# Kernel tuning notes

Hardware: AMD Instinct MI355X
Metric: run time of the kernel (lower is better)

## Reference

```python
import jax, jax.numpy as jnp
import numpy as np

N_NODES = 50000
N_EDGES = 800000
E_DIM = 128
N_LAYERS = 3
IN_DIM = 2
OUT_DIM = 1


def _lin_init(key, fan_in, fan_out, scale=None):
    # rough kaiming-tanh init, exact values don't matter for correctness testing
    s = scale if scale is not None else (5.0 / 3.0) / np.sqrt(fan_in)
    return jax.random.normal(key, (fan_in, fan_out), dtype=jnp.float32) * s


def setup_inputs() -> dict:
    key = jax.random.key(0)
    ks = jax.random.split(key, 16)
    node_feature = jax.random.normal(ks[0], (N_NODES, IN_DIM), dtype=jnp.float32)
    edge_index = jax.random.randint(ks[1], (2, N_EDGES), 0, N_NODES)
    batch = jnp.zeros((N_NODES,), dtype=jnp.int32)

    enc_W = _lin_init(ks[2], IN_DIM, E_DIM)
    enc_b = jnp.zeros((E_DIM,), dtype=jnp.float32)

    def stack(k, fan_in, fan_out):
        kk = jax.random.split(k, N_LAYERS)
        return jnp.stack([_lin_init(kk[i], fan_in, fan_out) for i in range(N_LAYERS)])

    gate_W = stack(ks[3], E_DIM, E_DIM)
    gate_b = jnp.zeros((N_LAYERS, E_DIM), dtype=jnp.float32)
    att_W = stack(ks[4], E_DIM, E_DIM)
    att_b = jnp.zeros((N_LAYERS, E_DIM), dtype=jnp.float32)
    msg_W = stack(ks[5], E_DIM, E_DIM)
    msg_b = jnp.zeros((N_LAYERS, E_DIM), dtype=jnp.float32)
    upd_W = stack(ks[6], 2 * E_DIM, E_DIM)
    upd_b = jnp.zeros((N_LAYERS, E_DIM), dtype=jnp.float32)

    dec1_W = _lin_init(ks[7], E_DIM, E_DIM // 2)
    dec1_b = jnp.zeros((E_DIM // 2,), dtype=jnp.float32)
    dec2_W = _lin_init(ks[8], E_DIM // 2, OUT_DIM, scale=1.0 / np.sqrt(E_DIM // 2))
    dec2_b = jnp.zeros((OUT_DIM,), dtype=jnp.float32)

    return dict(node_feature=node_feature, edge_index=edge_index, batch=batch,
                enc_W=enc_W, enc_b=enc_b,
                gate_W=gate_W, gate_b=gate_b, att_W=att_W, att_b=att_b,
                msg_W=msg_W, msg_b=msg_b, upd_W=upd_W, upd_b=upd_b,
                dec1_W=dec1_W, dec1_b=dec1_b, dec2_W=dec2_W, dec2_b=dec2_b)


def _segment_softmax(x, seg, num_segments):
    # PyG softmax over segments, numerically stable, per-channel
    m = jax.ops.segment_max(x, seg, num_segments=num_segments)
    m = jnp.where(jnp.isfinite(m), m, 0.0)
    e = jnp.exp(x - m[seg])
    s = jax.ops.segment_sum(e, seg, num_segments=num_segments)
    return e / (s[seg] + 1e-16)


def reference(node_feature, edge_index, batch,
              enc_W, enc_b, gate_W, gate_b, att_W, att_b,
              msg_W, msg_b, upd_W, upd_b,
              dec1_W, dec1_b, dec2_W, dec2_b):
    n = node_feature.shape[0]
    src, dst = edge_index[0], edge_index[1]  # j -> i (source_to_target)
    h = jnp.tanh(node_feature @ enc_W + enc_b)  # [N, E_DIM]
    for l in range(N_LAYERS):
        mj = jnp.tanh(h[src] @ msg_W[l] + msg_b[l])          # messages [Edges, E_DIM]
        gate = mj @ gate_W[l] + gate_b[l]                     # gate_nn (Linear only)
        alpha = _segment_softmax(gate, dst, n)                # softmax over incoming edges
        v = jnp.tanh(mj @ att_W[l] + att_b[l])                # attention_mlp
        aggr = jax.ops.segment_sum(alpha * v, dst, num_segments=n)
        h = jnp.tanh(jnp.concatenate([h, aggr], axis=1) @ upd_W[l] + upd_b[l])
    out = jnp.tanh(h @ dec1_W + dec1_b)
    out = out @ dec2_W + dec2_b
    return out
```

## Files before the change

kernel.cpp:

```cpp
#include <hip/hip_runtime.h>
#include <math.h>

#define ED 128
#define PROW 256

typedef _Float16 f16;
typedef _Float16 half8 __attribute__((ext_vector_type(8)));
typedef _Float16 half4 __attribute__((ext_vector_type(4)));
typedef _Float16 half2v __attribute__((ext_vector_type(2)));
typedef float f32x4 __attribute__((ext_vector_type(4)));

static __device__ __forceinline__ float tanh_fast(float x) {
  float ax = fabsf(x);
  float e = __expf(2.0f * ax);
  float t = 1.0f - 2.0f / (e + 1.0f);
  return __builtin_copysignf(t, x);
}

template <int NT, int NBYTES>
static __device__ __forceinline__ void stage256(
    const char* __restrict__ gsrc, char* lds, int tid) {
  #pragma unroll
  for (int i = 0; i < NBYTES / (NT * 16); ++i) {
    int b = (i * NT + tid) * 16;
    int row = b >> 8;
    int sw = (b & 255) ^ ((row & 7) << 4);
    float4 v = *reinterpret_cast<const float4*>(gsrc + (size_t)row * 256 + sw);
    *reinterpret_cast<float4*>(lds + b) = v;
  }
}

static __device__ __forceinline__ half8 read_w(const char* Wsb, int col, int koff) {
  int byte = col * 256 + (koff ^ ((col & 7) << 4));
  return *reinterpret_cast<const half8*>(Wsb + byte);
}

template <int NT>
static __device__ __forceinline__ void stage512(
    const char* __restrict__ gsrc, char* lds, int tid) {
  #pragma unroll
  for (int i = 0; i < 32768 / (NT * 16); ++i) {
    int b = (i * NT + tid) * 16;
    int row = b >> 9;
    int sw = (b & 511) ^ ((row & 7) << 4);
    float4 v = *reinterpret_cast<const float4*>(gsrc + (size_t)row * 512 + sw);
    *reinterpret_cast<float4*>(lds + b) = v;
  }
}

static __device__ __forceinline__ half8 read_w512(const char* Wsb, int colL, int koff) {
  int byte = colL * 512 + (koff ^ ((colL & 7) << 4));
  return *reinterpret_cast<const half8*>(Wsb + byte);
}

__global__ __launch_bounds__(256) void encoder_kernel(
    const float* __restrict__ x, const float* __restrict__ W,
    const float* __restrict__ b, f16* __restrict__ h, int n) {
  int idx = blockIdx.x * blockDim.x + threadIdx.x;
  if (idx >= n * ED) return;
  int i = idx >> 7, c = idx & 127;
  float v = x[i * 2 + 0] * W[c] + x[i * 2 + 1] * W[ED + c] + b[c];
  h[idx] = (f16)tanh_fast(v);
}

__global__ __launch_bounds__(256) void transpose_w_kernel(
    const float* __restrict__ src, f16* __restrict__ dst, int K, int C, int total) {
  int idx = blockIdx.x * 256 + threadIdx.x;
  if (idx >= total) return;
  int kc = K * C;
  int m = idx / kc;
  int rem = idx - m * kc;
  int c = rem / K;
  int k = rem - c * K;
  dst[idx] = (f16)src[(size_t)m * kc + (size_t)k * C + c];
}

__global__ __launch_bounds__(256) void transpose3_kernel(
    const float* __restrict__ s0, const float* __restrict__ s1,
    const float* __restrict__ s2, f16* __restrict__ d0,
    f16* __restrict__ d1, f16* __restrict__ d2) {
  int idx = blockIdx.x * 256 + threadIdx.x;
  const int per = 3 * 128 * 128;
  int which = idx / per;
  if (which >= 3) return;
  int rem = idx - which * per;
  const float* s = (which == 0) ? s0 : (which == 1) ? s1 : s2;
  f16* d = (which == 0) ? d0 : (which == 1) ? d1 : d2;
  int m = rem >> 14;
  int r2 = rem & 16383;
  int c = r2 >> 7, k = r2 & 127;
  d[rem] = (f16)s[m * 16384 + k * 128 + c];
}

__global__ __launch_bounds__(256) void count_deg_kernel(
    const int* __restrict__ dst, int* __restrict__ deg, int E) {
  int e = blockIdx.x * blockDim.x + threadIdx.x;
  if (e < E) atomicAdd(&deg[dst[e]], 1);
}

__global__ __launch_bounds__(1024) void scan_kernel(
    const int* __restrict__ deg, int* __restrict__ offs,
    int* __restrict__ cursor, int n) {
  __shared__ int wsum[16];
  __shared__ int carry_s;
  const int tid = threadIdx.x;
  const int lane = tid & 63;
  const int wid = tid >> 6;
  if (tid == 0) carry_s = 0;
  __syncthreads();
  for (int base = 0; base < n; base += 1024) {
    const int i = base + tid;
    const int v = (i < n) ? deg[i] : 0;
    int x = v;
    #pragma unroll
    for (int d = 1; d < 64; d <<= 1) {
      int t = __shfl_up(x, d, 64);
      if (lane >= d) x += t;
    }
    if (lane == 63) wsum[wid] = x;
    __syncthreads();
    int wbase = 0, total = 0;
    #pragma unroll
    for (int w = 0; w < 16; ++w) {
      int s = wsum[w];
      if (w < wid) wbase += s;
      total += s;
    }
    const int carry = carry_s;
    if (i < n) {
      const int excl = carry + wbase + x - v;
      offs[i] = excl;
      cursor[i] = excl;
    }
    __syncthreads();
    if (tid == 0) carry_s = carry + total;
    __syncthreads();
  }
  if (tid == 0) offs[n] = carry_s;
}

__global__ __launch_bounds__(256) void scatter_kernel(
    const int* __restrict__ src, const int* __restrict__ dst,
    int* __restrict__ cursor, int* __restrict__ ssrc, int E) {
  int e = blockIdx.x * blockDim.x + threadIdx.x;
  if (e < E) {
    int d = dst[e];
    int pos = atomicAdd(&cursor[d], 1);
    ssrc[pos] = src[e];
  }
}


__global__ __launch_bounds__(512, 4) void gemm_mgv_kernel(
    const f16* __restrict__ h,
    const f16* __restrict__ mWt, const float* __restrict__ mb,
    const f16* __restrict__ gWt, const float* __restrict__ gb,
    const f16* __restrict__ aWt, const float* __restrict__ ab,
    f16* __restrict__ P, int n) {
  __shared__ f16 Ws[128 * 128];
  __shared__ f16 Ss[128 * 128];
  char* Wsb = reinterpret_cast<char*>(Ws);
  char* Sb = reinterpret_cast<char*>(Ss);
  const int tid = threadIdx.x;
  const int wd = tid >> 6, lane = tid & 63;
  const int lr = lane & 15, lg = lane >> 4;
  const int r0 = blockIdx.x * 128 + wd * 16;

  half8 a[4];
  {
    int rr = r0 + lr;
    if (rr >= n) rr = n - 1;
    const f16* ap = h + (size_t)rr * ED + lg * 8;
    #pragma unroll
    for (int kt = 0; kt < 4; ++kt)
      a[kt] = *reinterpret_cast<const half8*>(ap + kt * 32);
  }

  stage256<512, 32768>((const char*)mWt, Wsb, tid);
  __syncthreads();
  #pragma unroll
  for (int t = 0; t < 8; ++t) {
    f32x4 acc = {0.f, 0.f, 0.f, 0.f};
    int col = t * 16 + lr;
    #pragma unroll
    for (int kt = 0; kt < 4; ++kt)
      acc = __builtin_amdgcn_mfma_f32_16x16x32_f16(a[kt], read_w(Wsb, col, lg * 16 + kt * 64), acc, 0, 0, 0);
    float bias = mb[col];
    #pragma unroll
    for (int j = 0; j < 4; ++j) {
      int srow = wd * 16 + lg * 4 + j;
      int byte = srow * 256 + (((col * 2) ^ ((srow & 7) << 4)));
      *reinterpret_cast<f16*>(Sb + byte) = (f16)tanh_fast(acc[j] + bias);
    }
  }
  half8 ma[4];
  {
    int lrow = wd * 16 + lr;
    #pragma unroll
    for (int kt = 0; kt < 4; ++kt) {
      int byte = lrow * 256 + ((lg * 16 + kt * 64) ^ ((lrow & 7) << 4));
      ma[kt] = *reinterpret_cast<const half8*>(Sb + byte);
    }
  }
  __syncthreads();

  stage256<512, 32768>((const char*)aWt, Wsb, tid);
  __syncthreads();
  half4 tq[8];
  #pragma unroll
  for (int t = 0; t < 8; ++t) {
    f32x4 acc = {0.f, 0.f, 0.f, 0.f};
    int col = t * 16 + lr;
    #pragma unroll
    for (int kt = 0; kt < 4; ++kt)
      acc = __builtin_amdgcn_mfma_f32_16x16x32_f16(ma[kt], read_w(Wsb, col, lg * 16 + kt * 64), acc, 0, 0, 0);
    float bias = ab[col];
    #pragma unroll
    for (int j = 0; j < 4; ++j) tq[t][j] = (f16)tanh_fast(acc[j] + bias);
  }
  __syncthreads();

  stage256<512, 32768>((const char*)gWt, Wsb, tid);
  __syncthreads();
  #pragma unroll
  for (int t = 0; t < 8; ++t) {
    f32x4 acc = {0.f, 0.f, 0.f, 0.f};
    int col = t * 16 + lr;
    #pragma unroll
    for (int kt = 0; kt < 4; ++kt)
      acc = __builtin_amdgcn_mfma_f32_16x16x32_f16(ma[kt], read_w(Wsb, col, lg * 16 + kt * 64), acc, 0, 0, 0);
    float bias = gb[col];
    #pragma unroll
    for (int j = 0; j < 4; ++j) {
      int grow = r0 + lg * 4 + j;
      if (grow < n) {
        float wexp = fminf(__expf(acc[j] + bias), 60000.f);
        half2v pr;
        pr.x = (f16)wexp;
        pr.y = (f16)(wexp * (float)tq[t][j]);
        *reinterpret_cast<half2v*>(P + (size_t)grow * PROW + col * 2) = pr;
      }
    }
  }
}

__global__ __launch_bounds__(512, 4) void updmgv_kernel(
    const f16* __restrict__ h, const f16* __restrict__ ag,
    const f16* __restrict__ uWt, const float* __restrict__ ub,
    const f16* __restrict__ mWt, const float* __restrict__ mb,
    const f16* __restrict__ gWt, const float* __restrict__ gb,
    const f16* __restrict__ aWt, const float* __restrict__ ab,
    f16* __restrict__ hout, f16* __restrict__ P, int n) {
  __shared__ f16 Ws[128 * 128];
  __shared__ f16 Ss[128 * 128];
  char* Wsb = reinterpret_cast<char*>(Ws);
  char* Sb = reinterpret_cast<char*>(Ss);
  const int tid = threadIdx.x;
  const int wd = tid >> 6, lane = tid & 63;
  const int lr = lane & 15, lg = lane >> 4;
  const int r0 = blockIdx.x * 128 + wd * 16;

  half8 ah[4], aa[4];
  {
    int rr = r0 + lr;
    if (rr >= n) rr = n - 1;
    const f16* ap = h + (size_t)rr * ED + lg * 8;
    const f16* bp = ag + (size_t)rr * ED + lg * 8;
    #pragma unroll
    for (int kt = 0; kt < 4; ++kt) {
      ah[kt] = *reinterpret_cast<const half8*>(ap + kt * 32);
      aa[kt] = *reinterpret_cast<const half8*>(bp + kt * 32);
    }
  }

  #pragma unroll
  for (int half = 0; half < 2; ++half) {
    __syncthreads();
    stage512<512>((const char*)uWt + (size_t)half * 64 * 512, Wsb, tid);
    __syncthreads();
    #pragma unroll
    for (int t = 0; t < 4; ++t) {
      int colL = t * 16 + lr;
      int col = half * 64 + colL;
      f32x4 acc = {0.f, 0.f, 0.f, 0.f};
      #pragma unroll
      for (int kt = 0; kt < 4; ++kt)
        acc = __builtin_amdgcn_mfma_f32_16x16x32_f16(ah[kt], read_w512(Wsb, colL, lg * 16 + kt * 64), acc, 0, 0, 0);
      #pragma unroll
      for (int kt = 0; kt < 4; ++kt)
        acc = __builtin_amdgcn_mfma_f32_16x16x32_f16(aa[kt], read_w512(Wsb, colL, 256 + lg * 16 + kt * 64), acc, 0, 0, 0);
      float bias = ub[col];
      #pragma unroll
      for (int j = 0; j < 4; ++j) {
        f16 hv = (f16)tanh_fast(acc[j] + bias);
        int srow = wd * 16 + lg * 4 + j;
        int byte = srow * 256 + (((col * 2) ^ ((srow & 7) << 4)));
        *reinterpret_cast<f16*>(Sb + byte) = hv;
        int grow = r0 + lg * 4 + j;
        if (grow < n) hout[(size_t)grow * ED + col] = hv;
      }
    }
  }
  half8 ha[4];
  {
    int lrow = wd * 16 + lr;
    #pragma unroll
    for (int kt = 0; kt < 4; ++kt) {
      int byte = lrow * 256 + ((lg * 16 + kt * 64) ^ ((lrow & 7) << 4));
      ha[kt] = *reinterpret_cast<const half8*>(Sb + byte);
    }
  }
  __syncthreads();

  stage256<512, 32768>((const char*)mWt, Wsb, tid);
  __syncthreads();
  #pragma unroll
  for (int t = 0; t < 8; ++t) {
    f32x4 acc = {0.f, 0.f, 0.f, 0.f};
    int col = t * 16 + lr;
    #pragma unroll
    for (int kt = 0; kt < 4; ++kt)
      acc = __builtin_amdgcn_mfma_f32_16x16x32_f16(ha[kt], read_w(Wsb, col, lg * 16 + kt * 64), acc, 0, 0, 0);
    float bias = mb[col];
    #pragma unroll
    for (int j = 0; j < 4; ++j) {
      int srow = wd * 16 + lg * 4 + j;
      int byte = srow * 256 + (((col * 2) ^ ((srow & 7) << 4)));
      *reinterpret_cast<f16*>(Sb + byte) = (f16)tanh_fast(acc[j] + bias);
    }
  }
  half8 ma[4];
  {
    int lrow = wd * 16 + lr;
    #pragma unroll
    for (int kt = 0; kt < 4; ++kt) {
      int byte = lrow * 256 + ((lg * 16 + kt * 64) ^ ((lrow & 7) << 4));
      ma[kt] = *reinterpret_cast<const half8*>(Sb + byte);
    }
  }
  __syncthreads();

  stage256<512, 32768>((const char*)aWt, Wsb, tid);
  __syncthreads();
  half4 tq[8];
  #pragma unroll
  for (int t = 0; t < 8; ++t) {
    f32x4 acc = {0.f, 0.f, 0.f, 0.f};
    int col = t * 16 + lr;
    #pragma unroll
    for (int kt = 0; kt < 4; ++kt)
      acc = __builtin_amdgcn_mfma_f32_16x16x32_f16(ma[kt], read_w(Wsb, col, lg * 16 + kt * 64), acc, 0, 0, 0);
    float bias = ab[col];
    #pragma unroll
    for (int j = 0; j < 4; ++j) tq[t][j] = (f16)tanh_fast(acc[j] + bias);
  }
  __syncthreads();

  stage256<512, 32768>((const char*)gWt, Wsb, tid);
  __syncthreads();
  #pragma unroll
  for (int t = 0; t < 8; ++t) {
    f32x4 acc = {0.f, 0.f, 0.f, 0.f};
    int col = t * 16 + lr;
    #pragma unroll
    for (int kt = 0; kt < 4; ++kt)
      acc = __builtin_amdgcn_mfma_f32_16x16x32_f16(ma[kt], read_w(Wsb, col, lg * 16 + kt * 64), acc, 0, 0, 0);
    float bias = gb[col];
    #pragma unroll
    for (int j = 0; j < 4; ++j) {
      int grow = r0 + lg * 4 + j;
      if (grow < n) {
        float wexp = fminf(__expf(acc[j] + bias), 60000.f);
        half2v pr;
        pr.x = (f16)wexp;
        pr.y = (f16)(wexp * (float)tq[t][j]);
        *reinterpret_cast<half2v*>(P + (size_t)grow * PROW + col * 2) = pr;
      }
    }
  }
}

__global__ __launch_bounds__(512, 4) void upddec_kernel(
    const f16* __restrict__ h, const f16* __restrict__ ag,
    const f16* __restrict__ uWt, const float* __restrict__ ub,
    const f16* __restrict__ d1Wt, const float* __restrict__ d1b,
    const float* __restrict__ d2W, const float* __restrict__ d2b,
    float* __restrict__ out, int n) {
  __shared__ f16 Ws[128 * 128];
  __shared__ f16 Ss[128 * 128];
  char* Wsb = reinterpret_cast<char*>(Ws);
  char* Sb = reinterpret_cast<char*>(Ss);
  const int tid = threadIdx.x;
  const int wd = tid >> 6, lane = tid & 63;
  const int lr = lane & 15, lg = lane >> 4;
  const int r0 = blockIdx.x * 128 + wd * 16;

  half8 ah[4], aa[4];
  {
    int rr = r0 + lr;
    if (rr >= n) rr = n - 1;
    const f16* ap = h + (size_t)rr * ED + lg * 8;
    const f16* bp = ag + (size_t)rr * ED + lg * 8;
    #pragma unroll
    for (int kt = 0; kt < 4; ++kt) {
      ah[kt] = *reinterpret_cast<const half8*>(ap + kt * 32);
      aa[kt] = *reinterpret_cast<const half8*>(bp + kt * 32);
    }
  }

  #pragma unroll
  for (int half = 0; half < 2; ++half) {
    __syncthreads();
    stage512<512>((const char*)uWt + (size_t)half * 64 * 512, Wsb, tid);
    __syncthreads();
    #pragma unroll
    for (int t = 0; t < 4; ++t) {
      int colL = t * 16 + lr;
      int col = half * 64 + colL;
      f32x4 acc = {0.f, 0.f, 0.f, 0.f};
      #pragma unroll
      for (int kt = 0; kt < 4; ++kt)
        acc = __builtin_amdgcn_mfma_f32_16x16x32_f16(ah[kt], read_w512(Wsb, colL, lg * 16 + kt * 64), acc, 0, 0, 0);
      #pragma unroll
      for (int kt = 0; kt < 4; ++kt)
        acc = __builtin_amdgcn_mfma_f32_16x16x32_f16(aa[kt], read_w512(Wsb, colL, 256 + lg * 16 + kt * 64), acc, 0, 0, 0);
      float bias = ub[col];
      #pragma unroll
      for (int j = 0; j < 4; ++j) {
        int srow = wd * 16 + lg * 4 + j;
        int byte = srow * 256 + (((col * 2) ^ ((srow & 7) << 4)));
        *reinterpret_cast<f16*>(Sb + byte) = (f16)tanh_fast(acc[j] + bias);
      }
    }
  }
  half8 ha[4];
  {
    int lrow = wd * 16 + lr;
    #pragma unroll
    for (int kt = 0; kt < 4; ++kt) {
      int byte = lrow * 256 + ((lg * 16 + kt * 64) ^ ((lrow & 7) << 4));
      ha[kt] = *reinterpret_cast<const half8*>(Sb + byte);
    }
  }
  __syncthreads();

  stage256<512, 16384>((const char*)d1Wt, Wsb, tid);
  __syncthreads();
  float rowsum[4] = {0.f, 0.f, 0.f, 0.f};
  #pragma unroll
  for (int t = 0; t < 4; ++t) {
    f32x4 acc = {0.f, 0.f, 0.f, 0.f};
    int col = t * 16 + lr;
    #pragma unroll
    for (int kt = 0; kt < 4; ++kt)
      acc = __builtin_amdgcn_mfma_f32_16x16x32_f16(ha[kt], read_w(Wsb, col, lg * 16 + kt * 64), acc, 0, 0, 0);
    float b1 = d1b[col], w2 = d2W[col];
    #pragma unroll
    for (int j = 0; j < 4; ++j) rowsum[j] += tanh_fast(acc[j] + b1) * w2;
  }
  #pragma unroll
  for (int d = 1; d < 16; d <<= 1) {
    #pragma unroll
    for (int j = 0; j < 4; ++j) rowsum[j] += __shfl_xor(rowsum[j], d, 64);
  }
  if (lr == 0) {
    #pragma unroll
    for (int j = 0; j < 4; ++j) {
      int grow = r0 + lg * 4 + j;
      if (grow < n) out[grow] = rowsum[j] + d2b[0];
    }
  }
}

__global__ __launch_bounds__(256) void edge_aggr_kernel(
    const int* __restrict__ offs, const int* __restrict__ ssrc,
    const f16* __restrict__ P, f16* __restrict__ aggr, int n) {
  int i = blockIdx.x * 4 + (threadIdx.x >> 6);
  if (i >= n) return;
  int lane = threadIdx.x & 63;
  int s0 = offs[i], s1 = offs[i + 1];
  const char* Pb = reinterpret_cast<const char*>(P);

  float sw0 = 0.f, wv0 = 0.f, sw1 = 0.f, wv1 = 0.f;
  #pragma unroll 4
  for (int e = s0; e < s1; ++e) {
    int sn = ssrc[e];
    half4 x = *reinterpret_cast<const half4*>(Pb + (size_t)sn * 512 + lane * 8);
    sw0 += (float)x.x;
    wv0 += (float)x.y;
    sw1 += (float)x.z;
    wv1 += (float)x.w;
  }
  half2v o;
  o.x = (f16)(wv0 / (sw0 + 1e-16f));
  o.y = (f16)(wv1 / (sw1 + 1e-16f));
  *reinterpret_cast<half2v*>(
      reinterpret_cast<char*>(aggr) + (size_t)i * 256 + (size_t)lane * 4) = o;
}

extern "C" void kernel_launch(void* const* d_in, const int* in_sizes, int n_in,
                              void* d_out, int out_size, void* d_ws, size_t ws_size,
                              hipStream_t stream) {
  const float* node_feature = (const float*)d_in[0];
  const int*   edge_index   = (const int*)d_in[1];
  const float* enc_W  = (const float*)d_in[3];
  const float* enc_b  = (const float*)d_in[4];
  const float* gate_W = (const float*)d_in[5];
  const float* gate_b = (const float*)d_in[6];
  const float* att_W  = (const float*)d_in[7];
  const float* att_b  = (const float*)d_in[8];
  const float* msg_W  = (const float*)d_in[9];
  const float* msg_b  = (const float*)d_in[10];
  const float* upd_W  = (const float*)d_in[11];
  const float* upd_b  = (const float*)d_in[12];
  const float* dec1_W = (const float*)d_in[13];
  const float* dec1_b = (const float*)d_in[14];
  const float* dec2_W = (const float*)d_in[15];
  const float* dec2_b = (const float*)d_in[16];

  const int n = in_sizes[0] / 2;
  const int E = in_sizes[1] / 2;
  const int* src = edge_index;
  const int* dst = edge_index + E;

  char* ws = (char*)d_ws;
  size_t off = 0;
  auto alloc = [&](size_t bytes) -> void* {
    void* p = ws + off;
    off += (bytes + 255) & ~(size_t)255;
    return p;
  };
  f16* hA   = (f16*)alloc((size_t)n * ED * 2);
  f16* hB   = (f16*)alloc((size_t)n * ED * 2);
  f16* P    = (f16*)alloc((size_t)n * PROW * 2);
  f16* aggr = (f16*)alloc((size_t)n * ED * 2);
  int* deg    = (int*)alloc((size_t)n * 4);
  int* offs   = (int*)alloc((size_t)(n + 1) * 4);
  int* cursor = (int*)alloc((size_t)n * 4);
  int* ssrc   = (int*)alloc((size_t)E * 4);
  f16* msgT  = (f16*)alloc((size_t)3 * ED * ED * 2);
  f16* gateT = (f16*)alloc((size_t)3 * ED * ED * 2);
  f16* attT  = (f16*)alloc((size_t)3 * ED * ED * 2);
  f16* updT  = (f16*)alloc((size_t)3 * ED * 2 * ED * 2);
  f16* dec1T = (f16*)alloc((size_t)ED * 64 * 2);

  {
    int tot3 = 3 * 3 * ED * ED;
    transpose3_kernel<<<(tot3 + 255) / 256, 256, 0, stream>>>(
        msg_W, gate_W, att_W, msgT, gateT, attT);
    int totu = 3 * 2 * ED * ED;
    transpose_w_kernel<<<(totu + 255) / 256, 256, 0, stream>>>(
        upd_W, updT, 2 * ED, ED, totu);
    int totd = ED * 64;
    transpose_w_kernel<<<(totd + 255) / 256, 256, 0, stream>>>(
        dec1_W, dec1T, ED, 64, totd);
  }

  hipMemsetAsync(deg, 0, (size_t)n * 4, stream);
  count_deg_kernel<<<(E + 255) / 256, 256, 0, stream>>>(dst, deg, E);
  scan_kernel<<<1, 1024, 0, stream>>>(deg, offs, cursor, n);
  scatter_kernel<<<(E + 255) / 256, 256, 0, stream>>>(src, dst, cursor, ssrc, E);

  encoder_kernel<<<((size_t)n * ED + 255) / 256, 256, 0, stream>>>(
      node_feature, enc_W, enc_b, hA, n);

  const int gemm_grid = (n + 127) / 128;
  const int aggr_grid = (n + 3) / 4;

  gemm_mgv_kernel<<<gemm_grid, 512, 0, stream>>>(
      hA, msgT, msg_b, gateT, gate_b, attT, att_b, P, n);
  edge_aggr_kernel<<<aggr_grid, 256, 0, stream>>>(offs, ssrc, P, aggr, n);

  updmgv_kernel<<<gemm_grid, 512, 0, stream>>>(
      hA, aggr, updT, upd_b,
      msgT + (size_t)1 * ED * ED, msg_b + ED,
      gateT + (size_t)1 * ED * ED, gate_b + ED,
      attT + (size_t)1 * ED * ED, att_b + ED,
      hB, P, n);
  edge_aggr_kernel<<<aggr_grid, 256, 0, stream>>>(offs, ssrc, P, aggr, n);

  updmgv_kernel<<<gemm_grid, 512, 0, stream>>>(
      hB, aggr, updT + (size_t)1 * 2 * ED * ED, upd_b + ED,
      msgT + (size_t)2 * ED * ED, msg_b + 2 * ED,
      gateT + (size_t)2 * ED * ED, gate_b + 2 * ED,
      attT + (size_t)2 * ED * ED, att_b + 2 * ED,
      hA, P, n);
  edge_aggr_kernel<<<aggr_grid, 256, 0, stream>>>(offs, ssrc, P, aggr, n);

  upddec_kernel<<<gemm_grid, 512, 0, stream>>>(
      hA, aggr, updT + (size_t)2 * 2 * ED * ED, upd_b + 2 * ED,
      dec1T, dec1_b, dec2_W, dec2_b, (float*)d_out, n);
}
```

Before: 447.2 us.

## Split P buffer into channel-group planes for cache-local edge gather

New measurement: 504.8 us. 12.9% more time.

```diff
diff --git a/kernel.cpp b/kernel.cpp
--- a/kernel.cpp
+++ b/kernel.cpp
@@ -2,7 +2,6 @@
 #include <math.h>
 
 #define ED 128
-#define PROW 256
 
 typedef _Float16 f16;
 typedef _Float16 half8 __attribute__((ext_vector_type(8)));
@@ -165,6 +164,7 @@
   const int wd = tid >> 6, lane = tid & 63;
   const int lr = lane & 15, lg = lane >> 4;
   const int r0 = blockIdx.x * 128 + wd * 16;
+  const size_t gstride = (size_t)n * 32;
 
   half8 a[4];
   {
@@ -238,7 +238,7 @@
         half2v pr;
         pr.x = (f16)wexp;
         pr.y = (f16)(wexp * (float)tq[t][j]);
-        *reinterpret_cast<half2v*>(P + (size_t)grow * PROW + col * 2) = pr;
+        *reinterpret_cast<half2v*>(P + (size_t)t * gstride + (size_t)grow * 32 + lr * 2) = pr;
       }
     }
   }
@@ -259,6 +259,7 @@
   const int wd = tid >> 6, lane = tid & 63;
   const int lr = lane & 15, lg = lane >> 4;
   const int r0 = blockIdx.x * 128 + wd * 16;
+  const size_t gstride = (size_t)n * 32;
 
   half8 ah[4], aa[4];
   {
@@ -374,7 +375,7 @@
         half2v pr;
         pr.x = (f16)wexp;
         pr.y = (f16)(wexp * (float)tq[t][j]);
-        *reinterpret_cast<half2v*>(P + (size_t)grow * PROW + col * 2) = pr;
+        *reinterpret_cast<half2v*>(P + (size_t)t * gstride + (size_t)grow * 32 + lr * 2) = pr;
       }
     }
   }
@@ -475,27 +476,25 @@
 __global__ __launch_bounds__(256) void edge_aggr_kernel(
     const int* __restrict__ offs, const int* __restrict__ ssrc,
     const f16* __restrict__ P, f16* __restrict__ aggr, int n) {
-  int i = blockIdx.x * 4 + (threadIdx.x >> 6);
-  if (i >= n) return;
+  int g = blockIdx.x & 7;
+  int nb = blockIdx.x >> 3;
   int lane = threadIdx.x & 63;
-  int s0 = offs[i], s1 = offs[i + 1];
-  const char* Pb = reinterpret_cast<const char*>(P);
-
-  float sw0 = 0.f, wv0 = 0.f, sw1 = 0.f, wv1 = 0.f;
+  int sub = lane >> 4;
+  int ch = lane & 15;
+  int node = nb * 16 + (threadIdx.x >> 6) * 4 + sub;
+  if (node >= n) return;
+  const f16* Pg = P + (size_t)g * (size_t)n * 32;
+  int s0 = offs[node], s1 = offs[node + 1];
+
+  float sw = 0.f, swv = 0.f;
   #pragma unroll 4
   for (int e = s0; e < s1; ++e) {
     int sn = ssrc[e];
-    half4 x = *reinterpret_cast<const half4*>(Pb + (size_t)sn * 512 + lane * 8);
-    sw0 += (float)x.x;
-    wv0 += (float)x.y;
-    sw1 += (float)x.z;
-    wv1 += (float)x.w;
-  }
-  half2v o;
-  o.x = (f16)(wv0 / (sw0 + 1e-16f));
-  o.y = (f16)(wv1 / (sw1 + 1e-16f));
-  *reinterpret_cast<half2v*>(
-      reinterpret_cast<char*>(aggr) + (size_t)i * 256 + (size_t)lane * 4) = o;
+    half2v x = *reinterpret_cast<const half2v*>(Pg + (size_t)sn * 32 + ch * 2);
+    sw += (float)x.x;
+    swv += (float)x.y;
+  }
+  aggr[(size_t)node * ED + g * 16 + ch] = (f16)(swv / (sw + 1e-16f));
 }
 
 extern "C" void kernel_launch(void* const* d_in, const int* in_sizes, int n_in,
@@ -532,7 +531,7 @@
   };
   f16* hA   = (f16*)alloc((size_t)n * ED * 2);
   f16* hB   = (f16*)alloc((size_t)n * ED * 2);
-  f16* P    = (f16*)alloc((size_t)n * PROW * 2);
+  f16* P    = (f16*)alloc((size_t)n * 256 * 2);
   f16* aggr = (f16*)alloc((size_t)n * ED * 2);
   int* deg    = (int*)alloc((size_t)n * 4);
   int* offs   = (int*)alloc((size_t)(n + 1) * 4);
@@ -565,7 +564,7 @@
       node_feature, enc_W, enc_b, hA, n);
 
   const int gemm_grid = (n + 127) / 128;
-  const int aggr_grid = (n + 3) / 4;
+  const int aggr_grid = ((n + 15) / 16) * 8;
 
   gemm_mgv_kernel<<<gemm_grid, 512, 0, stream>>>(
       hA, msgT, msg_b, gateT, gate_b, attT, att_b, P, n);
```
